# Performance work log

Measured on AMD Instinct MI355X. Metric: run time of the kernel, lower is better.

The kernel has to match this reference:

```python
import jax, jax.numpy as jnp
import numpy as np

N = 128          # preconditioner matrix dim = 8*8*2
L8 = 8           # lattice extent
KAPPA = 0.276
MAXITER = 20
NENT = N * (N + 1) // 2  # 8256 lower-triangular entries
_rows, _cols = np.tril_indices(N)

G = [jnp.array([[0, 1], [1, 0]], dtype=jnp.complex64),          # gamma_1 = sigma_x
     jnp.array([[0, -1j], [1j, 0]], dtype=jnp.complex64)]        # gamma_2 = sigma_y
I2 = jnp.eye(2, dtype=jnp.complex64)


def _D(x, U):
    # Wilson-Dirac: x (B,8,8,2) spinor field, U (B,2,8,8) complex links.
    out = x
    for mu in range(2):
        ax = mu + 1
        Um = U[:, mu]                                  # U_mu(n)
        Umb = jnp.roll(jnp.conj(Um), 1, axis=ax)       # U_mu^dag(n-mu)
        fwd = Um[..., None] * jnp.roll(x, -1, axis=ax)  # U(n) x(n+mu)
        bwd = Umb[..., None] * jnp.roll(x, 1, axis=ax)  # U^dag(n-mu) x(n-mu)
        out = out - KAPPA * (jnp.einsum('st,bxyt->bxys', I2 - G[mu], fwd)
                             + jnp.einsum('st,bxyt->bxys', I2 + G[mu], bwd))
    return out


def _Ddag(y, U):
    # Adjoint of _D: projectors swap on forward/backward hops.
    out = y
    for mu in range(2):
        ax = mu + 1
        Um = U[:, mu]
        Umb = jnp.roll(jnp.conj(Um), 1, axis=ax)
        fwd = Um[..., None] * jnp.roll(y, -1, axis=ax)
        bwd = Umb[..., None] * jnp.roll(y, 1, axis=ax)
        out = out - KAPPA * (jnp.einsum('st,bxyt->bxys', I2 + G[mu], fwd)
                             + jnp.einsum('st,bxyt->bxys', I2 - G[mu], bwd))
    return out


def setup_inputs() -> dict:
    key = jax.random.key(0)
    k1, k2, k3, k4 = jax.random.split(key, 4)
    B = 2048
    return {
        'net_out_re': jax.random.normal(k1, (B, NENT), jnp.float32),
        'net_out_im': jax.random.normal(k2, (B, NENT), jnp.float32),
        'theta': jax.random.normal(k3, (B, 2, L8, L8), jnp.float32),
        'b': jax.random.uniform(k4, (B, L8, L8, 2), jnp.float32),
    }


def reference(net_out_re, net_out_im, theta, b):
    net_out = (net_out_re + 1j * net_out_im).astype(jnp.complex64)  # (B, 8256)
    U = jnp.exp(1j * theta).astype(jnp.complex64)                   # (B, 2, 8, 8)
    bc = b.astype(jnp.complex64)                                    # (B, 8, 8, 2)
    B = bc.shape[0]

    # Dense lower-triangular factor (scatter of net_out, as in upper_tri_mat).
    Lmat = jnp.zeros((B, N, N), jnp.complex64).at[:, _rows, _cols].set(net_out)

    def M(x):  # preconditioner: L^H (L v)
        v = x.reshape(B, -1)
        w = jnp.einsum('bij,bj->bi', Lmat, v)
        u = jnp.einsum('bji,bj->bi', jnp.conj(Lmat), w)
        return u.reshape(x.shape)

    def A(x):  # DDOpt = D^dag D (Hermitian PSD)
        return _Ddag(_D(x, U), U)

    def dot(a, c):  # batched complex inner product
        return jnp.sum(jnp.conj(a) * c, axis=(1, 2, 3), keepdims=True)

    x0 = jnp.zeros_like(bc)
    r = bc - A(x0)
    z = M(r)
    p = z
    rz = dot(r, z)

    def step(carry, _):
        x, r, p, rz = carry
        Ap = A(p)
        alpha = rz / dot(p, Ap)
        x = x + alpha * p
        r = r - alpha * Ap
        z = M(r)
        rz2 = dot(r, z)
        p = z + (rz2 / rz) * p
        return (x, r, p, rz2), None

    (x, _, _, _), _ = jax.lax.scan(step, (x0, r, p, rz), None, length=MAXITER)

    res = A(x) - bc
    rn = jnp.linalg.norm(res.reshape(B, -1), axis=1)  # real per-batch norms
    return jnp.mean(rn).astype(jnp.float32)
```

## Files before the change

### kernel.cpp

```cpp
#include <hip/hip_runtime.h>
#include <math.h>

#define NV 128
#define NTRI 8256
#define NPAD8R 8960
#define KAP 0.276f
#define MAXIT 20
#define TPB 512

__device__ __forceinline__ float2 f2(float x, float y){ return make_float2(x, y); }
__device__ __forceinline__ float2 cadd(float2 a, float2 b){ return make_float2(a.x+b.x, a.y+b.y); }
__device__ __forceinline__ float2 csub(float2 a, float2 b){ return make_float2(a.x-b.x, a.y-b.y); }
__device__ __forceinline__ float2 cmul(float2 a, float2 b){ return make_float2(a.x*b.x - a.y*b.y, a.x*b.y + a.y*b.x); }
__device__ __forceinline__ float2 cmulc(float2 a, float2 b){
  return make_float2(a.x*b.x + a.y*b.y, a.x*b.y - a.y*b.x); }
__device__ __forceinline__ float2 cmac(float2 acc, float2 a, float2 b){
  acc.x = fmaf(a.x, b.x, fmaf(-a.y, b.y, acc.x));
  acc.y = fmaf(a.x, b.y, fmaf( a.y, b.x, acc.y));
  return acc; }
__device__ __forceinline__ float2 cmacc(float2 acc, float2 a, float2 b){
  acc.x = fmaf(a.x, b.x, fmaf( a.y, b.y, acc.x));
  acc.y = fmaf(a.x, b.y, fmaf(-a.y, b.x, acc.y));
  return acc; }
__device__ __forceinline__ float2 cdiv(float2 n, float2 d){
  float s = 1.0f / fmaf(d.x, d.x, d.y*d.y);
  return make_float2((n.x*d.x + n.y*d.y)*s, (n.y*d.x - n.x*d.y)*s); }

__device__ __forceinline__ int soff8(int r){
  const int a = r >> 3;
  return ((((a + 1) * ((a << 2) + (r & 7)))) << 3) + (r << 1);
}
__device__ __forceinline__ int skey(int r){ return ((r >> 1) & 3) << 1; }

__device__ __forceinline__ float2 red8(float2 v){
  v.x += __shfl_xor(v.x, 1);  v.y += __shfl_xor(v.y, 1);
  v.x += __shfl_xor(v.x, 2);  v.y += __shfl_xor(v.y, 2);
  v.x += __shfl_xor(v.x, 32); v.y += __shfl_xor(v.y, 32);
  return v;
}

template<int EF>
__device__ __forceinline__ void dirac(const float2* __restrict__ U,
                                      const float2* __restrict__ vin,
                                      float2* __restrict__ vout, int t)
{
  if (t < NV) {
    const int s = t & 1, site = t >> 1;
    const int yi = site & 7, xi = site >> 3;
    const int xp = (xi+1)&7, xm = (xi-1)&7, yp = (yi+1)&7, ym = (yi-1)&7;
    float2 acc;
    {
      const int bf = (xp<<4) + (yi<<1);
      float2 fs = vin[bf + s], fo = vin[bf + (s^1)];
      float2 cf = (EF > 0) ? cadd(fs, fo) : csub(fs, fo);
      acc = cmul(U[(xi<<3)+yi], cf);
      const int bb = (xm<<4) + (yi<<1);
      float2 bs = vin[bb + s], bo = vin[bb + (s^1)];
      float2 cb = (EF > 0) ? csub(bs, bo) : cadd(bs, bo);
      acc = cadd(acc, cmulc(U[(xm<<3)+yi], cb));
    }
    {
      const float tg = s ? 1.0f : -1.0f;
      const float gf = (float)EF * tg;
      const int bf = (xi<<4) + (yp<<1);
      float2 fs = vin[bf + s], fo = vin[bf + (s^1)];
      float2 cf = make_float2(fmaf(-gf, fo.y, fs.x), fmaf(gf, fo.x, fs.y));
      acc = cadd(acc, cmul(U[64 + (xi<<3)+yi], cf));
      const float gb = -gf;
      const int bb = (xi<<4) + (ym<<1);
      float2 bs = vin[bb + s], bo = vin[bb + (s^1)];
      float2 cb = make_float2(fmaf(-gb, bo.y, bs.x), fmaf(gb, bo.x, bs.y));
      acc = cadd(acc, cmulc(U[64 + (xi<<3)+ym], cb));
    }
    float2 v0 = vin[t];
    vout[t] = make_float2(fmaf(-KAP, acc.x, v0.x), fmaf(-KAP, acc.y, v0.y));
  }
  __syncthreads();
}

__device__ __forceinline__ void precond(const float2* __restrict__ Lc2,
                                        const float2* __restrict__ vin,
                                        float2* __restrict__ wvv,
                                        float2* __restrict__ vout,
                                        int w, int lane)
{
  const int c  = lane & 3;
  const int g  = lane >> 2;
  const int q  = g & 7;
  const int h  = g >> 3;
  const int c2 = c << 1;
  const int rlo = (w << 3) + q;
  const int rhi = 127 - rlo;
  const int bLo = soff8(rlo);
  const int bHi = soff8(rhi);
  const int keyLo = skey(rlo);
  const int keyHi = skey(rhi);

  {
    float2 a0 = f2(0.f, 0.f), a1 = f2(0.f, 0.f);
    #pragma unroll
    for (int i = 0; i < 8; ++i) {
      if (i <= w) {
        const int k    = h ? (8 - w + i) : i;
        const int base = h ? bHi : bLo;
        const int keyR = h ? keyHi : keyLo;
        const float4 Lp = *(const float4*)&Lc2[base + (k << 3) + c2];
        const float4 vp = *(const float4*)&vin[(k << 3) + (c2 ^ keyR)];
        a0 = cmac(cmac(a0, f2(Lp.x,Lp.y), f2(vp.x,vp.y)), f2(Lp.z,Lp.w), f2(vp.z,vp.w));
      } else {
        const int k  = h ? (8 - w + i) : (i - w - 1);
        const float4 Lp = *(const float4*)&Lc2[bHi + (k << 3) + c2];
        const float4 vp = *(const float4*)&vin[(k << 3) + (c2 ^ keyHi)];
        a1 = cmac(cmac(a1, f2(Lp.x,Lp.y), f2(vp.x,vp.y)), f2(Lp.z,Lp.w), f2(vp.z,vp.w));
      }
    }
    if (!h) {
      const int k = 7 - w;
      const float4 Lp = *(const float4*)&Lc2[bHi + (k << 3) + c2];
      const float4 vp = *(const float4*)&vin[(k << 3) + (c2 ^ keyHi)];
      a1 = cmac(cmac(a1, f2(Lp.x,Lp.y), f2(vp.x,vp.y)), f2(Lp.z,Lp.w), f2(vp.z,vp.w));
    }
    float2 vLo = h ? f2(0.f, 0.f) : a0;
    float2 vHi = h ? cadd(a0, a1) : a1;
    vLo = red8(vLo);
    vHi = red8(vHi);
    if (c == 0) wvv[h ? rhi : rlo] = h ? vHi : vLo;
  }
  __syncthreads();

  {
    const int key2 = c2;
    float2 a0 = f2(0.f, 0.f), a1 = f2(0.f, 0.f);
    #pragma unroll
    for (int i = 0; i < 8; ++i) {
      int k, j;
      if (i <= w) {
        k = h ? (8 + i) : (15 - w + i);
        j = h ? rlo : rhi;
      } else {
        k = h ? (8 + i) : (i - 1);
        j = rlo;
      }
      const int u    = (k + 1) << 3;
      const int off0 = u * ((k << 2) + c2) + (k << 4) + (c2 << 1) + (j ^ key2);
      const int off1 = off0 + u + 2;
      const int i0   = (k << 3) + c2;
      const float2 La = Lc2[off0];
      const float2 Lb = Lc2[off1];
      const float4 wp = *(const float4*)&wvv[i0];
      if (i <= w) a0 = cmacc(cmacc(a0, La, f2(wp.x,wp.y)), Lb, f2(wp.z,wp.w));
      else        a1 = cmacc(cmacc(a1, La, f2(wp.x,wp.y)), Lb, f2(wp.z,wp.w));
    }
    if (!h) {
      const int o0 = (64 * (28 + c2)) + 112 + (c2 << 1) + (rlo ^ key2);
      const float2 La = Lc2[o0];
      const float2 Lb = Lc2[o0 + 66];
      const float4 wp = *(const float4*)&wvv[56 + c2];
      a1 = cmacc(cmacc(a1, La, f2(wp.x,wp.y)), Lb, f2(wp.z,wp.w));
    }
    float2 vJhi = h ? f2(0.f, 0.f) : a0;
    float2 vJlo = h ? cadd(a0, a1) : a1;
    vJhi = red8(vJhi);
    vJlo = red8(vJlo);
    if (c == 0) vout[h ? rlo : rhi] = h ? vJlo : vJhi;
  }
  __syncthreads();
}

__device__ __forceinline__ float2 block_dot(const float2* __restrict__ a, const float2* __restrict__ c,
                            float2* __restrict__ scal, int t, int slot)
{
  if (t < NV) {
    float2 v = cmacc(f2(0.f,0.f), a[t], c[t]);
    #pragma unroll
    for (int off = 32; off > 0; off >>= 1) {
      v.x += __shfl_down(v.x, off, 64);
      v.y += __shfl_down(v.y, off, 64);
    }
    if ((t & 63) == 0) scal[(slot<<1) + (t >> 6)] = v;
  }
  __syncthreads();
  return cadd(scal[slot<<1], scal[(slot<<1)+1]);
}

extern "C" __global__ void __launch_bounds__(TPB, 4)
cg_loss_kernel(const float* __restrict__ nre, const float* __restrict__ nim,
               const float* __restrict__ theta, const float* __restrict__ bin,
               float* __restrict__ out, float invB)
{
  __shared__ __align__(16) float2 Lc2[NPAD8R];
  __shared__ __align__(16) float2 Uc[128];
  __shared__ __align__(16) float2 bv[NV], xv[NV], rv[NV], pv[NV];
  __shared__ __align__(16) float2 zv[NV], Apv[NV], tv[NV], wv[NV];
  __shared__ float2 scal[8];

  const int t = threadIdx.x;
  const long long b = blockIdx.x;
  const int w = t >> 6, lane = t & 63;

  for (int p = t; p < NPAD8R; p += TPB) Lc2[p] = make_float2(0.f, 0.f);
  if (t < NV) {
    float th = theta[b * 128 + t];
    float sn, cs;
    sincosf(th, &sn, &cs);
    Uc[t] = make_float2(cs, sn);
    float bb = bin[b * 128 + t];
    bv[t] = make_float2(bb, 0.f);
    xv[t] = make_float2(0.f, 0.f);
    rv[t] = make_float2(bb, 0.f);
  }
  __syncthreads();

  {
    const float* nreb = nre + b * NTRI;
    const float* nimb = nim + b * NTRI;
    for (int p = t; p < NTRI; p += TPB) {
      float re = nreb[p], im = nimb[p];
      int r = (int)((sqrtf(8.f * (float)p + 1.f) - 1.f) * 0.5f + 1e-3f);
      int tr = (r * (r + 1)) >> 1;
      if (tr > p)               { tr -= r; --r; }
      else if (tr + r + 1 <= p) { tr += r + 1; ++r; }
      Lc2[soff8(r) + ((p - tr) ^ skey(r))] = make_float2(re, im);
    }
  }
  __syncthreads();

  precond(Lc2, rv, wv, zv, w, lane);
  if (t < NV) pv[t] = zv[t];
  float2 rz = block_dot(rv, zv, scal, t, 0);

  #pragma unroll 1
  for (int it = 0; it < MAXIT; ++it) {
    dirac<-1>(Uc, pv, tv, t);
    dirac<+1>(Uc, tv, Apv, t);
    float2 pAp = block_dot(pv, Apv, scal, t, 1);
    if (t < NV) {
      float2 alpha = cdiv(rz, pAp);
      xv[t] = cmac(xv[t], alpha, pv[t]);
      rv[t] = csub(rv[t], cmul(alpha, Apv[t]));
    }
    __syncthreads();
    precond(Lc2, rv, wv, zv, w, lane);
    float2 rz2 = block_dot(rv, zv, scal, t, 0);
    if (t < NV) {
      float2 beta = cdiv(rz2, rz);
      pv[t] = cmac(zv[t], beta, pv[t]);
    }
    rz = rz2;
    __syncthreads();
  }

  dirac<-1>(Uc, xv, tv, t);
  dirac<+1>(Uc, tv, Apv, t);
  if (t < NV) {
    float2 d = csub(Apv[t], bv[t]);
    float v = fmaf(d.x, d.x, d.y * d.y);
    #pragma unroll
    for (int off = 32; off > 0; off >>= 1) v += __shfl_down(v, off, 64);
    if ((t & 63) == 0) scal[4 + (t >> 6)].x = v;
  }
  __syncthreads();
  if (t == 0) {
    float rn = sqrtf(scal[4].x + scal[5].x);
    atomicAdd(out, rn * invB);
  }
}

extern "C" void kernel_launch(void* const* d_in, const int* in_sizes, int n_in,
                              void* d_out, int out_size, void* d_ws, size_t ws_size,
                              hipStream_t stream)
{
  const float* nre   = (const float*)d_in[0];
  const float* nim   = (const float*)d_in[1];
  const float* theta = (const float*)d_in[2];
  const float* bin   = (const float*)d_in[3];
  float* out = (float*)d_out;
  const int B = in_sizes[0] / NTRI;

  hipMemsetAsync(out, 0, sizeof(float), stream);
  cg_loss_kernel<<<B, TPB, 0, stream>>>(nre, nim, theta, bin, out, 1.0f / (float)B);
}
```

Baseline: 514.1 us.

## Keep CG vectors in registers and fuse dot products into Dirac and preconditioner

Moves x, r, p and the CG scalars into per-thread registers and computes the second Dirac application directly into registers. The p·Ap reduction is fused into that Dirac step and r·z into the preconditioner's output stage. The final iteration is peeled so it skips the unused residual and preconditioner work. Together these remove several __syncthreads barriers and shared-memory round trips per CG iteration, at the cost of more register pressure and more complex control flow.

```diff
diff --git a/kernel.cpp b/kernel.cpp
--- a/kernel.cpp
+++ b/kernel.cpp
@@ -40,41 +40,46 @@
 }
 
 template<int EF>
+__device__ __forceinline__ float2 dirac_reg(const float2* __restrict__ U,
+                                            const float2* __restrict__ vin, int t)
+{
+  const int s = t & 1, site = t >> 1;
+  const int yi = site & 7, xi = site >> 3;
+  const int xp = (xi+1)&7, xm = (xi-1)&7, yp = (yi+1)&7, ym = (yi-1)&7;
+  float2 acc;
+  {
+    const int bf = (xp<<4) + (yi<<1);
+    float2 fs = vin[bf + s], fo = vin[bf + (s^1)];
+    float2 cf = (EF > 0) ? cadd(fs, fo) : csub(fs, fo);
+    acc = cmul(U[(xi<<3)+yi], cf);
+    const int bb = (xm<<4) + (yi<<1);
+    float2 bs = vin[bb + s], bo = vin[bb + (s^1)];
+    float2 cb = (EF > 0) ? csub(bs, bo) : cadd(bs, bo);
+    acc = cadd(acc, cmulc(U[(xm<<3)+yi], cb));
+  }
+  {
+    const float tg = s ? 1.0f : -1.0f;
+    const float gf = (float)EF * tg;
+    const int bf = (xi<<4) + (yp<<1);
+    float2 fs = vin[bf + s], fo = vin[bf + (s^1)];
+    float2 cf = make_float2(fmaf(-gf, fo.y, fs.x), fmaf(gf, fo.x, fs.y));
+    acc = cadd(acc, cmul(U[64 + (xi<<3)+yi], cf));
+    const float gb = -gf;
+    const int bb = (xi<<4) + (ym<<1);
+    float2 bs = vin[bb + s], bo = vin[bb + (s^1)];
+    float2 cb = make_float2(fmaf(-gb, bo.y, bs.x), fmaf(gb, bo.x, bs.y));
+    acc = cadd(acc, cmulc(U[64 + (xi<<3)+ym], cb));
+  }
+  float2 v0 = vin[t];
+  return make_float2(fmaf(-KAP, acc.x, v0.x), fmaf(-KAP, acc.y, v0.y));
+}
+
+template<int EF>
 __device__ __forceinline__ void dirac(const float2* __restrict__ U,
                                       const float2* __restrict__ vin,
                                       float2* __restrict__ vout, int t)
 {
-  if (t < NV) {
-    const int s = t & 1, site = t >> 1;
-    const int yi = site & 7, xi = site >> 3;
-    const int xp = (xi+1)&7, xm = (xi-1)&7, yp = (yi+1)&7, ym = (yi-1)&7;
-    float2 acc;
-    {
-      const int bf = (xp<<4) + (yi<<1);
-      float2 fs = vin[bf + s], fo = vin[bf + (s^1)];
-      float2 cf = (EF > 0) ? cadd(fs, fo) : csub(fs, fo);
-      acc = cmul(U[(xi<<3)+yi], cf);
-      const int bb = (xm<<4) + (yi<<1);
-      float2 bs = vin[bb + s], bo = vin[bb + (s^1)];
-      float2 cb = (EF > 0) ? csub(bs, bo) : cadd(bs, bo);
-      acc = cadd(acc, cmulc(U[(xm<<3)+yi], cb));
-    }
-    {
-      const float tg = s ? 1.0f : -1.0f;
-      const float gf = (float)EF * tg;
-      const int bf = (xi<<4) + (yp<<1);
-      float2 fs = vin[bf + s], fo = vin[bf + (s^1)];
-      float2 cf = make_float2(fmaf(-gf, fo.y, fs.x), fmaf(gf, fo.x, fs.y));
-      acc = cadd(acc, cmul(U[64 + (xi<<3)+yi], cf));
-      const float gb = -gf;
-      const int bb = (xi<<4) + (ym<<1);
-      float2 bs = vin[bb + s], bo = vin[bb + (s^1)];
-      float2 cb = make_float2(fmaf(-gb, bo.y, bs.x), fmaf(gb, bo.x, bs.y));
-      acc = cadd(acc, cmulc(U[64 + (xi<<3)+ym], cb));
-    }
-    float2 v0 = vin[t];
-    vout[t] = make_float2(fmaf(-KAP, acc.x, v0.x), fmaf(-KAP, acc.y, v0.y));
-  }
+  if (t < NV) vout[t] = dirac_reg<EF>(U, vin, t);
   __syncthreads();
 }
 
@@ -82,6 +87,7 @@
                                         const float2* __restrict__ vin,
                                         float2* __restrict__ wvv,
                                         float2* __restrict__ vout,
+                                        float2* __restrict__ scal,
                                         int w, int lane)
 {
   const int c  = lane & 3;
@@ -162,25 +168,21 @@
     float2 vJlo = h ? cadd(a0, a1) : a1;
     vJhi = red8(vJhi);
     vJlo = red8(vJlo);
-    if (c == 0) vout[h ? rlo : rhi] = h ? vJlo : vJhi;
-  }
-  __syncthreads();
-}
-
-__device__ __forceinline__ float2 block_dot(const float2* __restrict__ a, const float2* __restrict__ c,
-                            float2* __restrict__ scal, int t, int slot)
-{
-  if (t < NV) {
-    float2 v = cmacc(f2(0.f,0.f), a[t], c[t]);
+    float2 dotp = f2(0.f, 0.f);
+    if (c == 0) {
+      const int jw = h ? rlo : rhi;
+      const float2 zj = h ? vJlo : vJhi;
+      vout[jw] = zj;
+      dotp = cmacc(f2(0.f, 0.f), vin[jw], zj);
+    }
     #pragma unroll
-    for (int off = 32; off > 0; off >>= 1) {
-      v.x += __shfl_down(v.x, off, 64);
-      v.y += __shfl_down(v.y, off, 64);
-    }
-    if ((t & 63) == 0) scal[(slot<<1) + (t >> 6)] = v;
-  }
-  __syncthreads();
-  return cadd(scal[slot<<1], scal[(slot<<1)+1]);
+    for (int off = 32; off >= 4; off >>= 1) {
+      dotp.x += __shfl_down(dotp.x, off, 64);
+      dotp.y += __shfl_down(dotp.y, off, 64);
+    }
+    if (lane == 0) scal[w] = dotp;
+  }
+  __syncthreads();
 }
 
 extern "C" __global__ void __launch_bounds__(TPB, 4)
@@ -190,15 +192,16 @@
 {
   __shared__ __align__(16) float2 Lc2[NPAD8R];
   __shared__ __align__(16) float2 Uc[128];
-  __shared__ __align__(16) float2 bv[NV], xv[NV], rv[NV], pv[NV];
-  __shared__ __align__(16) float2 zv[NV], Apv[NV], tv[NV], wv[NV];
-  __shared__ float2 scal[8];
+  __shared__ __align__(16) float2 bv[NV], rv[NV], pv[NV];
+  __shared__ __align__(16) float2 zv[NV], tv[NV], wv[NV];
+  __shared__ float2 scal[12];
 
   const int t = threadIdx.x;
   const long long b = blockIdx.x;
   const int w = t >> 6, lane = t & 63;
 
   for (int p = t; p < NPAD8R; p += TPB) Lc2[p] = make_float2(0.f, 0.f);
+  float2 xr = f2(0.f, 0.f), rr = f2(0.f, 0.f), pr = f2(0.f, 0.f), rz = f2(1.f, 0.f);
   if (t < NV) {
     float th = theta[b * 128 + t];
     float sn, cs;
@@ -206,8 +209,8 @@
     Uc[t] = make_float2(cs, sn);
     float bb = bin[b * 128 + t];
     bv[t] = make_float2(bb, 0.f);
-    xv[t] = make_float2(0.f, 0.f);
-    rv[t] = make_float2(bb, 0.f);
+    rr = make_float2(bb, 0.f);
+    rv[t] = rr;
   }
   __syncthreads();
 
@@ -225,43 +228,83 @@
   }
   __syncthreads();
 
-  precond(Lc2, rv, wv, zv, w, lane);
-  if (t < NV) pv[t] = zv[t];
-  float2 rz = block_dot(rv, zv, scal, t, 0);
+  precond(Lc2, rv, wv, zv, scal, w, lane);
+  if (t < NV) {
+    rz = cadd(cadd(cadd(scal[0],scal[1]), cadd(scal[2],scal[3])),
+              cadd(cadd(scal[4],scal[5]), cadd(scal[6],scal[7])));
+    pr = zv[t];
+    pv[t] = pr;
+  }
+  __syncthreads();
 
   #pragma unroll 1
-  for (int it = 0; it < MAXIT; ++it) {
+  for (int it = 0; it < MAXIT - 1; ++it) {
     dirac<-1>(Uc, pv, tv, t);
-    dirac<+1>(Uc, tv, Apv, t);
-    float2 pAp = block_dot(pv, Apv, scal, t, 1);
-    if (t < NV) {
-      float2 alpha = cdiv(rz, pAp);
-      xv[t] = cmac(xv[t], alpha, pv[t]);
-      rv[t] = csub(rv[t], cmul(alpha, Apv[t]));
-    }
-    __syncthreads();
-    precond(Lc2, rv, wv, zv, w, lane);
-    float2 rz2 = block_dot(rv, zv, scal, t, 0);
-    if (t < NV) {
+    float2 ap = f2(0.f, 0.f);
+    if (t < NV) {
+      ap = dirac_reg<+1>(Uc, tv, t);
+      float2 v = cmacc(f2(0.f,0.f), pr, ap);
+      #pragma unroll
+      for (int off = 32; off > 0; off >>= 1) {
+        v.x += __shfl_down(v.x, off, 64);
+        v.y += __shfl_down(v.y, off, 64);
+      }
+      if ((t & 63) == 0) scal[8 + (t >> 6)] = v;
+    }
+    __syncthreads();
+    if (t < NV) {
+      float2 alpha = cdiv(rz, cadd(scal[8], scal[9]));
+      xr = cmac(xr, alpha, pr);
+      rr = csub(rr, cmul(alpha, ap));
+      rv[t] = rr;
+    }
+    __syncthreads();
+    precond(Lc2, rv, wv, zv, scal, w, lane);
+    if (t < NV) {
+      float2 rz2 = cadd(cadd(cadd(scal[0],scal[1]), cadd(scal[2],scal[3])),
+                        cadd(cadd(scal[4],scal[5]), cadd(scal[6],scal[7])));
       float2 beta = cdiv(rz2, rz);
-      pv[t] = cmac(zv[t], beta, pv[t]);
-    }
-    rz = rz2;
-    __syncthreads();
-  }
-
-  dirac<-1>(Uc, xv, tv, t);
-  dirac<+1>(Uc, tv, Apv, t);
+      rz = rz2;
+      pr = cmac(zv[t], beta, pr);
+      pv[t] = pr;
+    }
+    __syncthreads();
+  }
+
+  dirac<-1>(Uc, pv, tv, t);
+  {
+    float2 ap = f2(0.f, 0.f);
+    if (t < NV) {
+      ap = dirac_reg<+1>(Uc, tv, t);
+      float2 v = cmacc(f2(0.f,0.f), pr, ap);
+      #pragma unroll
+      for (int off = 32; off > 0; off >>= 1) {
+        v.x += __shfl_down(v.x, off, 64);
+        v.y += __shfl_down(v.y, off, 64);
+      }
+      if ((t & 63) == 0) scal[8 + (t >> 6)] = v;
+    }
+    __syncthreads();
+    if (t < NV) {
+      float2 alpha = cdiv(rz, cadd(scal[8], scal[9]));
+      xr = cmac(xr, alpha, pr);
+      rv[t] = xr;
+    }
+    __syncthreads();
+  }
+
+  dirac<-1>(Uc, rv, tv, t);
   if (t < NV) {
-    float2 d = csub(Apv[t], bv[t]);
+    float2 ax = dirac_reg<+1>(Uc, tv, t);
+    float2 d = csub(ax, bv[t]);
     float v = fmaf(d.x, d.x, d.y * d.y);
     #pragma unroll
     for (int off = 32; off > 0; off >>= 1) v += __shfl_down(v, off, 64);
-    if ((t & 63) == 0) scal[4 + (t >> 6)].x = v;
+    if ((t & 63) == 0) scal[10 + (t >> 6)].x = v;
   }
   __syncthreads();
   if (t == 0) {
-    float rn = sqrtf(scal[4].x + scal[5].x);
+    float rn = sqrtf(scal[10].x + scal[11].x);
     atomicAdd(out, rn * invB);
   }
 }
```

Measured after the change: 514.8 us. About the same (+0.1%).
